# Performance work log

Measured on AMD Instinct MI355X. Metric: run time of the kernel, lower is better.

## Reference

```python
import jax, jax.numpy as jnp
import numpy as np

# Acoustic FDTD constants (seistorch-style geometry)
NSHOTS, NT = 4, 512
NZ, NX = 256, 256
NRECS = 128
DT = 1e-3   # s
DH = 10.0   # m grid spacing


def setup_inputs() -> dict:
    key = jax.random.key(0)
    k1, k2, k3, k4, k5, k6 = jax.random.split(key, 6)
    x = jax.random.normal(k1, (NSHOTS, NT), dtype=jnp.float32)  # source wavelets
    # velocity model in [1500, 4000] m/s (CFL: dt*vmax/dh = 0.4 < stability limit)
    vp = 1500.0 + 2500.0 * jax.random.uniform(k2, (NZ, NX), dtype=jnp.float32)
    src_z = jax.random.randint(k3, (NSHOTS,), 0, NZ)
    src_x = jax.random.randint(k4, (NSHOTS,), 0, NX)
    rec_z = jax.random.randint(k5, (NSHOTS, NRECS), 0, NZ)
    rec_x = jax.random.randint(k6, (NSHOTS, NRECS), 0, NX)
    return {"x": x, "vp": vp, "src_z": src_z, "src_x": src_x,
            "rec_z": rec_z, "rec_x": rec_x}


def _laplacian(p):
    # 5-point stencil, zero Dirichlet boundary. p: (B, NZ, NX)
    pp = jnp.pad(p, ((0, 0), (1, 1), (1, 1)))
    return (pp[:, 2:, 1:-1] + pp[:, :-2, 1:-1]
            + pp[:, 1:-1, 2:] + pp[:, 1:-1, :-2]
            - 4.0 * p) / (DH * DH)


def reference(x, vp, src_z, src_x, rec_z, rec_x):
    shots = jnp.arange(NSHOTS)
    c2dt2 = (vp * DT) ** 2  # (NZ, NX), broadcast over shots

    def step(carry, wav_t):
        p_prev, p = carry
        # 2nd-order acoustic update (the PDE "cell")
        p_next = 2.0 * p - p_prev + c2dt2 * _laplacian(p)
        # source scatter-inject (super_source)
        p_next = p_next.at[shots, src_z, src_x].add(wav_t * DT * DT)
        # receiver gather (super_probes): (NSHOTS, NRECS)
        rec = p_next[shots[:, None], rec_z, rec_x]
        return (p, p_next), rec

    p0 = jnp.zeros((NSHOTS, NZ, NX), dtype=x.dtype)
    _, recs = jax.lax.scan(step, (p0, p0), x.T)  # recs: (NT, NSHOTS, NRECS)
    # (shots, time, receivers, n_receiver_types=1)
    return jnp.transpose(recs, (1, 0, 2))[..., None]
```

## Files before the change

kernel.cpp:

```cpp
#include <hip/hip_runtime.h>

#define NSHOTS 4
#define NT     512
#define NZ     256
#define NX     256
#define NRECS  128

static constexpr float DTf    = 0.001f;
static constexpr float INVDH2 = 1.0f / (10.0f * 10.0f);

#define KSTEPS 16
#define TILE   32
#define RPT    8
#define NPAIRS 4
#define NWAVES 8
#define BLOCK  512
#define NWG    (NSHOTS * 64)
#define NPHASE (NT / KSTEPS)
#define LSTRIDE 32

typedef float v2f __attribute__((ext_vector_type(2)));

__device__ __forceinline__ float nbr_left(float v) {
  return __int_as_float(__builtin_amdgcn_update_dpp(
      0, __float_as_int(v), 0x138 , 0xf, 0xf, true));
}
__device__ __forceinline__ float nbr_right(float v) {
  return __int_as_float(__builtin_amdgcn_update_dpp(
      0, __float_as_int(v), 0x130 , 0xf, 0xf, true));
}

__device__ __forceinline__ float gload(const float* p) {
  return __hip_atomic_load(p, __ATOMIC_RELAXED, __HIP_MEMORY_SCOPE_AGENT);
}
__device__ __forceinline__ void gstore(float* p, float v) {
  __hip_atomic_store(p, v, __ATOMIC_RELAXED, __HIP_MEMORY_SCOPE_AGENT);
}
__device__ __forceinline__ unsigned fload(const unsigned* p) {
  return __hip_atomic_load(p, __ATOMIC_RELAXED, __HIP_MEMORY_SCOPE_AGENT);
}
__device__ __forceinline__ void fstore(unsigned* p, unsigned v) {
  __hip_atomic_store(p, v, __ATOMIC_RELAXED, __HIP_MEMORY_SCOPE_AGENT);
}

__global__ __launch_bounds__(BLOCK, 4) void wave_pk(
    float* __restrict__ f0c, float* __restrict__ f0p,
    float* __restrict__ f1c, float* __restrict__ f1p,
    const float* __restrict__ vp, const float* __restrict__ xwav,
    const int* __restrict__ src_z, const int* __restrict__ src_x,
    const int* __restrict__ rec_z, const int* __restrict__ rec_x,
    float* __restrict__ out,
    unsigned* __restrict__ bar)
{
  const int bid  = blockIdx.x;
  const int s    = bid >> 6;
  const int tz   = (bid >> 3) & 7;
  const int tx   = bid & 7;
  const int tid  = threadIdx.x;
  const int w    = tid >> 6;
  const int lane = tid & 63;

  const int gz0 = tz * TILE - KSTEPS;
  const int gx0 = tx * TILE - KSTEPS;
  const int gx  = gx0 + lane;
  const int zb  = w * RPT;

  __shared__ float haloTop[2][NWAVES][64];
  __shared__ float haloBot[2][NWAVES][64];
  __shared__ float recTile[2][TILE][TILE + 1];
  __shared__ int   cntS;
  __shared__ int   lzA[NRECS], lxA[NRECS];
  __shared__ unsigned pkA[NRECS];

  if (tid == 0) cntS = 0;
  __syncthreads();
  if (tid < NRECS) {
    const int lz = rec_z[s * NRECS + tid] - tz * TILE;
    const int lx = rec_x[s * NRECS + tid] - tx * TILE;
    lzA[tid] = lz; lxA[tid] = lx;
    if ((unsigned)lz < (unsigned)TILE && (unsigned)lx < (unsigned)TILE) {
      const int k = atomicAdd(&cntS, 1);
      pkA[k] = (unsigned)tid | ((unsigned)lz << 8) | ((unsigned)lx << 16);
    }
  }
  __syncthreads();
  const int nRec = cntS;
  int myR = 0, myLz = 0, myLx = 0;
  if (tid < nRec) {
    const unsigned p = pkA[tid];
    myR = p & 255; myLz = (p >> 8) & 31; myLx = (p >> 16) & 31;
  }
  const bool wbRow = (w >= 2 && w < 6) && (lane >= KSTEPS && lane < KSTEPS + TILE);
  const int  ilz   = (w - 2) * RPT;
  const int  ilx   = lane - KSTEPS;
  unsigned recMask = 0;
  if (wbRow) {
    for (int r = 0; r < NRECS; ++r)
      if (lxA[r] == ilx && (unsigned)(lzA[r] - ilz) < (unsigned)RPT)
        recMask |= 1u << (lzA[r] - ilz);
  }

  int nb = -1;
  if (tid < 8) {
    const int k  = (tid < 4) ? tid : tid + 1;
    const int dz = k / 3 - 1, dx = k % 3 - 1;
    const int qz = tz + dz, qx = tx + dx;
    if ((unsigned)qz < 8u && (unsigned)qx < 8u)
      nb = (s << 6) | (qz << 3) | qx;
  }
  unsigned* wF = bar;

  auto pollGE = [&](unsigned* base, unsigned target) {
    if (nb >= 0) {
      while (fload(base + (size_t)nb * LSTRIDE) < target)
        __builtin_amdgcn_s_sleep(1);
    }
  };

  const int slz = src_z[s] - gz0;
  const int slx = src_x[s] - gx0;
  const bool srcMine = (slx == lane) && ((unsigned)(slz - zb) < (unsigned)RPT);
  const int  srcI = slz - zb;
  v2f srcM2[NPAIRS];
  #pragma unroll
  for (int p = 0; p < NPAIRS; ++p) {
    srcM2[p].x = (srcMine && srcI == 2 * p)     ? 1.0f : 0.0f;
    srcM2[p].y = (srcMine && srcI == 2 * p + 1) ? 1.0f : 0.0f;
  }

  const bool xok = (unsigned)gx < (unsigned)NX;
  int   offRow[RPT];
  bool  okRow[RPT];
  v2f a2[NPAIRS], b2[NPAIRS], c22[NPAIRS], d22[NPAIRS];
  #pragma unroll
  for (int p = 0; p < NPAIRS; ++p) {
    #pragma unroll
    for (int h = 0; h < 2; ++h) {
      const int i  = 2 * p + h;
      const int gz = gz0 + zb + i;
      const bool ok = xok && ((unsigned)gz < (unsigned)NZ);
      okRow[i]  = ok;
      offRow[i] = ok ? ((s * NZ + gz) * NX + gx) : 0;
      float v = ok ? vp[gz * NX + gx] : 0.0f;
      v *= DTf;
      const float c2 = v * v * INVDH2;
      if (h == 0) { c22[p].x = c2; d22[p].x = 2.0f - 4.0f * c2; }
      else        { c22[p].y = c2; d22[p].y = 2.0f - 4.0f * c2; }
    }
    a2[p] = (v2f)(0.0f); b2[p] = (v2f)(0.0f);
  }

  #pragma unroll 1
  for (int ph = 0; ph < NPHASE; ++ph) {
    const int t0 = ph * KSTEPS;

    float amp[KSTEPS];
    {
      const float4* xw4 = (const float4*)(xwav + s * NT + t0);
      #pragma unroll
      for (int q = 0; q < KSTEPS / 4; ++q) {
        const float4 v = xw4[q];
        amp[4 * q + 0] = (v.x * DTf) * DTf;
        amp[4 * q + 1] = (v.y * DTf) * DTf;
        amp[4 * q + 2] = (v.z * DTf) * DTf;
        amp[4 * q + 3] = (v.w * DTf) * DTf;
      }
    }

    if (ph > 0) {
      pollGE(wF, (unsigned)ph);
      __syncthreads();
      const float* rc = (ph & 1) ? f0c : f1c;
      const float* rp = (ph & 1) ? f0p : f1p;
      if (!wbRow) {
        #pragma unroll
        for (int p = 0; p < NPAIRS; ++p) {
          a2[p].x = okRow[2 * p]     ? gload(rc + offRow[2 * p])     : 0.0f;
          a2[p].y = okRow[2 * p + 1] ? gload(rc + offRow[2 * p + 1]) : 0.0f;
          b2[p].x = okRow[2 * p]     ? gload(rp + offRow[2 * p])     : 0.0f;
          b2[p].y = okRow[2 * p + 1] ? gload(rp + offRow[2 * p + 1]) : 0.0f;
        }
      }
    }

    float recv[KSTEPS];

    auto do_step = [&](v2f (&cur)[NPAIRS], v2f (&nxt)[NPAIRS], int tau) {
      const int pb = tau & 1;
      haloTop[pb][w][lane] = cur[0].x;
      haloBot[pb][w][lane] = cur[NPAIRS - 1].y;
      __syncthreads();
      if (tau > 0 && tid < nRec) recv[tau - 1] = recTile[1 - pb][myLz][myLx];
      const float up0 = (w > 0)          ? haloBot[pb][w - 1][lane] : 0.0f;
      const float dn7 = (w < NWAVES - 1) ? haloTop[pb][w + 1][lane] : 0.0f;
      const v2f av = { amp[tau], amp[tau] };
      #pragma unroll
      for (int p = 0; p < NPAIRS; ++p) {
        const float cx = cur[p].x, cy = cur[p].y;
        const float upx = (p == 0)          ? up0 : cur[p - 1].y;
        const float dny = (p == NPAIRS - 1) ? dn7 : cur[p + 1].x;
        v2f ud, lr;
        ud.x = upx + cy;
        ud.y = cx + dny;
        lr.x = nbr_left(cx) + nbr_right(cx);
        lr.y = nbr_left(cy) + nbr_right(cy);
        const v2f sum = ud + lr;
        v2f t = __builtin_elementwise_fma(c22[p], sum, -nxt[p]);
        t = __builtin_elementwise_fma(d22[p], cur[p], t);
        t = __builtin_elementwise_fma(srcM2[p], av, t);
        nxt[p] = t;
      }
      if (recMask) {
        #pragma unroll
        for (int i = 0; i < RPT; ++i)
          if (recMask & (1u << i))
            recTile[pb][ilz + i][ilx] = (i & 1) ? nxt[i >> 1].y : nxt[i >> 1].x;
      }
    };

    #pragma unroll
    for (int h = 0; h < KSTEPS / 2; ++h) {
      do_step(a2, b2, 2 * h);
      do_step(b2, a2, 2 * h + 1);
    }

    if (ph != NPHASE - 1) {
      float* wc = (ph & 1) ? f1c : f0c;
      float* wp = (ph & 1) ? f1p : f0p;
      if (wbRow) {
        #pragma unroll
        for (int p = 0; p < NPAIRS; ++p) {
          gstore(wc + offRow[2 * p],     a2[p].x);
          gstore(wc + offRow[2 * p + 1], a2[p].y);
          gstore(wp + offRow[2 * p],     b2[p].x);
          gstore(wp + offRow[2 * p + 1], b2[p].y);
        }
      }
      __builtin_amdgcn_s_waitcnt(0);
      __syncthreads();
      if (tid == 0) fstore(wF + (size_t)bid * LSTRIDE, (unsigned)(ph + 1));
    } else {
      __syncthreads();
    }

    if (tid < nRec) {
      recv[KSTEPS - 1] = recTile[1][myLz][myLx];
      #pragma unroll
      for (int t = 0; t < KSTEPS; ++t)
        out[(s * NT + (t0 + t)) * NRECS + myR] = recv[t];
    }
  }
}

extern "C" void kernel_launch(void* const* d_in, const int* in_sizes, int n_in,
                              void* d_out, int out_size, void* d_ws, size_t ws_size,
                              hipStream_t stream) {
  const float* x     = (const float*)d_in[0];
  const float* vp    = (const float*)d_in[1];
  const int*   src_z = (const int*)d_in[2];
  const int*   src_x = (const int*)d_in[3];
  const int*   rec_z = (const int*)d_in[4];
  const int*   rec_x = (const int*)d_in[5];
  float* out = (float*)d_out;

  float* ws = (float*)d_ws;
  const size_t F = (size_t)NSHOTS * NZ * NX;
  float* f0c = ws;
  float* f0p = ws + F;
  float* f1c = ws + 2 * F;
  float* f1p = ws + 3 * F;
  unsigned* bar = (unsigned*)(ws + 4 * F);

  hipMemsetAsync(bar, 0, (size_t)NWG * LSTRIDE * sizeof(unsigned), stream);

  wave_pk<<<dim3(NWG), dim3(BLOCK), 0, stream>>>(
      f0c, f0p, f1c, f1p, vp, x, src_z, src_x, rec_z, rec_x, out, bar);
}
```

Baseline: 317.6 us.

## Replace per-block flag barrier with tagged 64-bit data words for neighbor sync

Packs current and previous field values into one 64-bit word. A 2-bit phase tag goes in the low mantissa bits of the previous value. Readers spin on each word until its tag matches, which removes the separate flag array, the store waitcnt, the extra barriers and the flag polling. The cost is slightly lower precision on the previous field, a larger memset of the whole workspace each launch, and fine-grained polling traffic on the data itself.

New measurement: 303.8 us. 4.4% less time.

```diff
diff --git a/kernel.cpp b/kernel.cpp
--- a/kernel.cpp
+++ b/kernel.cpp
@@ -17,9 +17,9 @@
 #define BLOCK  512
 #define NWG    (NSHOTS * 64)
 #define NPHASE (NT / KSTEPS)
-#define LSTRIDE 32
 
 typedef float v2f __attribute__((ext_vector_type(2)));
+typedef unsigned long long ull;
 
 __device__ __forceinline__ float nbr_left(float v) {
   return __int_as_float(__builtin_amdgcn_update_dpp(
@@ -30,27 +30,33 @@
       0, __float_as_int(v), 0x130 , 0xf, 0xf, true));
 }
 
-__device__ __forceinline__ float gload(const float* p) {
+__device__ __forceinline__ ull pload(const ull* p) {
   return __hip_atomic_load(p, __ATOMIC_RELAXED, __HIP_MEMORY_SCOPE_AGENT);
 }
-__device__ __forceinline__ void gstore(float* p, float v) {
+__device__ __forceinline__ void pstore(ull* p, ull v) {
   __hip_atomic_store(p, v, __ATOMIC_RELAXED, __HIP_MEMORY_SCOPE_AGENT);
 }
-__device__ __forceinline__ unsigned fload(const unsigned* p) {
-  return __hip_atomic_load(p, __ATOMIC_RELAXED, __HIP_MEMORY_SCOPE_AGENT);
-}
-__device__ __forceinline__ void fstore(unsigned* p, unsigned v) {
-  __hip_atomic_store(p, v, __ATOMIC_RELAXED, __HIP_MEMORY_SCOPE_AGENT);
+
+__device__ __forceinline__ ull pack_w(float cur, float prev, unsigned tg) {
+  const unsigned hi = (__float_as_uint(prev) & ~3u) | tg;
+  return ((ull)hi << 32) | (ull)__float_as_uint(cur);
+}
+__device__ __forceinline__ float w_cur(ull w) {
+  return __uint_as_float((unsigned)w);
+}
+__device__ __forceinline__ float w_prev(ull w) {
+  return __uint_as_float(((unsigned)(w >> 32)) & ~3u);
+}
+__device__ __forceinline__ unsigned tag_of(int q) {
+  return ((unsigned)(q >> 1) % 3u) + 1u;
 }
 
 __global__ __launch_bounds__(BLOCK, 4) void wave_pk(
-    float* __restrict__ f0c, float* __restrict__ f0p,
-    float* __restrict__ f1c, float* __restrict__ f1p,
+    ull* __restrict__ gA, ull* __restrict__ gB,
     const float* __restrict__ vp, const float* __restrict__ xwav,
     const int* __restrict__ src_z, const int* __restrict__ src_x,
     const int* __restrict__ rec_z, const int* __restrict__ rec_x,
-    float* __restrict__ out,
-    unsigned* __restrict__ bar)
+    float* __restrict__ out)
 {
   const int bid  = blockIdx.x;
   const int s    = bid >> 6;
@@ -100,23 +106,6 @@
         recMask |= 1u << (lzA[r] - ilz);
   }
 
-  int nb = -1;
-  if (tid < 8) {
-    const int k  = (tid < 4) ? tid : tid + 1;
-    const int dz = k / 3 - 1, dx = k % 3 - 1;
-    const int qz = tz + dz, qx = tx + dx;
-    if ((unsigned)qz < 8u && (unsigned)qx < 8u)
-      nb = (s << 6) | (qz << 3) | qx;
-  }
-  unsigned* wF = bar;
-
-  auto pollGE = [&](unsigned* base, unsigned target) {
-    if (nb >= 0) {
-      while (fload(base + (size_t)nb * LSTRIDE) < target)
-        __builtin_amdgcn_s_sleep(1);
-    }
-  };
-
   const int slz = src_z[s] - gz0;
   const int slx = src_x[s] - gx0;
   const bool srcMine = (slx == lane) && ((unsigned)(slz - zb) < (unsigned)RPT);
@@ -132,6 +121,7 @@
   int   offRow[RPT];
   bool  okRow[RPT];
   v2f a2[NPAIRS], b2[NPAIRS], c22[NPAIRS], d22[NPAIRS];
+  unsigned okMask = 0;
   #pragma unroll
   for (int p = 0; p < NPAIRS; ++p) {
     #pragma unroll
@@ -140,6 +130,7 @@
       const int gz = gz0 + zb + i;
       const bool ok = xok && ((unsigned)gz < (unsigned)NZ);
       okRow[i]  = ok;
+      if (ok) okMask |= 1u << i;
       offRow[i] = ok ? ((s * NZ + gz) * NX + gx) : 0;
       float v = ok ? vp[gz * NX + gx] : 0.0f;
       v *= DTf;
@@ -167,19 +158,30 @@
       }
     }
 
-    if (ph > 0) {
-      pollGE(wF, (unsigned)ph);
-      __syncthreads();
-      const float* rc = (ph & 1) ? f0c : f1c;
-      const float* rp = (ph & 1) ? f0p : f1p;
-      if (!wbRow) {
-        #pragma unroll
-        for (int p = 0; p < NPAIRS; ++p) {
-          a2[p].x = okRow[2 * p]     ? gload(rc + offRow[2 * p])     : 0.0f;
-          a2[p].y = okRow[2 * p + 1] ? gload(rc + offRow[2 * p + 1]) : 0.0f;
-          b2[p].x = okRow[2 * p]     ? gload(rp + offRow[2 * p])     : 0.0f;
-          b2[p].y = okRow[2 * p + 1] ? gload(rp + offRow[2 * p + 1]) : 0.0f;
-        }
+    if (ph > 0 && !wbRow) {
+      const ull* gR = (ph & 1) ? gA : gB;
+      const unsigned tg = tag_of(ph - 1);
+      ull vw[RPT];
+      unsigned need = okMask;
+      while (need) {
+        ull t[RPT];
+        #pragma unroll
+        for (int i = 0; i < RPT; ++i)
+          if (need & (1u << i)) t[i] = pload(gR + offRow[i]);
+        #pragma unroll
+        for (int i = 0; i < RPT; ++i)
+          if ((need & (1u << i)) && (((unsigned)(t[i] >> 32)) & 3u) == tg) {
+            vw[i] = t[i];
+            need &= ~(1u << i);
+          }
+        if (need) __builtin_amdgcn_s_sleep(1);
+      }
+      #pragma unroll
+      for (int i = 0; i < RPT; ++i) {
+        const float cv = okRow[i] ? w_cur(vw[i])  : 0.0f;
+        const float pv = okRow[i] ? w_prev(vw[i]) : 0.0f;
+        if (i & 1) { a2[i >> 1].y = cv; b2[i >> 1].y = pv; }
+        else       { a2[i >> 1].x = cv; b2[i >> 1].x = pv; }
       }
     }
 
@@ -225,23 +227,17 @@
     }
 
     if (ph != NPHASE - 1) {
-      float* wc = (ph & 1) ? f1c : f0c;
-      float* wp = (ph & 1) ? f1p : f0p;
+      ull* gW = (ph & 1) ? gB : gA;
+      const unsigned tgw = tag_of(ph);
       if (wbRow) {
         #pragma unroll
         for (int p = 0; p < NPAIRS; ++p) {
-          gstore(wc + offRow[2 * p],     a2[p].x);
-          gstore(wc + offRow[2 * p + 1], a2[p].y);
-          gstore(wp + offRow[2 * p],     b2[p].x);
-          gstore(wp + offRow[2 * p + 1], b2[p].y);
+          pstore(gW + offRow[2 * p],     pack_w(a2[p].x, b2[p].x, tgw));
+          pstore(gW + offRow[2 * p + 1], pack_w(a2[p].y, b2[p].y, tgw));
         }
       }
-      __builtin_amdgcn_s_waitcnt(0);
-      __syncthreads();
-      if (tid == 0) fstore(wF + (size_t)bid * LSTRIDE, (unsigned)(ph + 1));
-    } else {
-      __syncthreads();
-    }
+    }
+    __syncthreads();
 
     if (tid < nRec) {
       recv[KSTEPS - 1] = recTile[1][myLz][myLx];
@@ -263,16 +259,12 @@
   const int*   rec_x = (const int*)d_in[5];
   float* out = (float*)d_out;
 
-  float* ws = (float*)d_ws;
   const size_t F = (size_t)NSHOTS * NZ * NX;
-  float* f0c = ws;
-  float* f0p = ws + F;
-  float* f1c = ws + 2 * F;
-  float* f1p = ws + 3 * F;
-  unsigned* bar = (unsigned*)(ws + 4 * F);
-
-  hipMemsetAsync(bar, 0, (size_t)NWG * LSTRIDE * sizeof(unsigned), stream);
+  ull* gA = (ull*)d_ws;
+  ull* gB = gA + F;
+
+  hipMemsetAsync(gA, 0, 2 * F * sizeof(ull), stream);
 
   wave_pk<<<dim3(NWG), dim3(BLOCK), 0, stream>>>(
-      f0c, f0p, f1c, f1p, vp, x, src_z, src_x, rec_z, rec_x, out, bar);
-}
+      gA, gB, vp, x, src_z, src_x, rec_z, rec_x, out);
+}
```
